# Kernel tuning notes

Measured on AMD Instinct MI355X. Metric: run time of the kernel, lower is better.

Reference implementation:

```python
import jax, jax.numpy as jnp
import numpy as np

B, L, D_IN, D_MODEL, N_LAYERS, D_STATE, D_OUT = 32, 1024, 3, 512, 4, 64, 10


def setup_inputs() -> dict:
    key = jax.random.key(0)
    ks = jax.random.split(key, 6)
    x = jax.random.normal(ks[0], (B, L, D_IN), jnp.float32)
    W_enc = jax.random.normal(ks[1], (D_IN, D_MODEL), jnp.float32) / np.sqrt(D_IN)
    # per-channel log timestep, standard S4 init range [1e-3, 1e-1]
    log_dt = jax.random.uniform(ks[2], (N_LAYERS, D_MODEL), jnp.float32,
                                minval=np.log(1e-3), maxval=np.log(1e-1))
    # S4D-real init: A_n = -(n + 1/2), stored as log of magnitude
    A_log = jnp.broadcast_to(
        jnp.log(0.5 + jnp.arange(D_STATE, dtype=jnp.float32)),
        (N_LAYERS, D_MODEL, D_STATE)) * jnp.ones((), jnp.float32)
    C = jax.random.normal(ks[3], (N_LAYERS, D_MODEL, D_STATE), jnp.float32) / np.sqrt(D_STATE)
    W_ff = jax.random.normal(ks[4], (N_LAYERS, D_MODEL, D_MODEL), jnp.float32) / np.sqrt(D_MODEL)
    W_dec = jax.random.normal(ks[5], (D_MODEL, D_OUT), jnp.float32) / np.sqrt(D_MODEL)
    return dict(x=x, W_enc=W_enc, log_dt=log_dt, A_log=A_log, C=C, W_ff=W_ff, W_dec=W_dec)


def _s4d(x, log_dt, A_log, C):
    """Diagonal real S4D layer (is_real=True, skip=False, identity activation).
    x: (B, L, H); log_dt: (H,); A_log, C: (H, N).
    """
    Lx = x.shape[1]
    dt = jnp.exp(log_dt)                         # (H,)
    A = -jnp.exp(A_log)                          # (H, N) real negative poles
    dtA = dt[:, None] * A                        # (H, N)
    Bbar = (jnp.exp(dtA) - 1.0) / A              # ZOH discretization with B = 1
    # Vandermonde kernel: K[h, l] = sum_n (C*Bbar)[h, n] * exp(dtA[h, n] * l)
    lrange = jnp.arange(Lx, dtype=x.dtype)
    K = jnp.einsum('hn,hnl->hl', C * Bbar, jnp.exp(dtA[:, :, None] * lrange))
    # causal depthwise convolution via FFT (linear conv, pad to 2L)
    n = 2 * Lx
    Kf = jnp.fft.rfft(K, n=n, axis=-1)           # (H, n//2+1)
    xf = jnp.fft.rfft(x, n=n, axis=1)            # (B, n//2+1, H)
    y = jnp.fft.irfft(xf * Kf.T[None], n=n, axis=1)[:, :Lx]
    return y


def reference(x, W_enc, log_dt, A_log, C, W_ff, W_dec):
    h = x @ W_enc                                # (B, L, d_model), bias=False
    for i in range(N_LAYERS):
        h = _s4d(h, log_dt[i], A_log[i], C[i])   # S4D layer
        # dropout is identity at inference; FF block: Linear(no bias) + ReLU
        h = jax.nn.relu(h @ W_ff[i])
    out = h @ W_dec                              # (B, L, d_output)
    return out[:, -1, :]                         # get_last=True -> (B, d_output)
```

## Files before the change

kernel.cpp:

```cpp
#include <hip/hip_runtime.h>
#include <math.h>

#define B_   32
#define L_   1024
#define BT_  (B_*L_)
#define DIN  3
#define H_   512
#define NL   4
#define NS   64
#define DOUT 10
#define CT   128
#define NC   (L_/CT)
#define BH   (B_*H_)

typedef __attribute__((ext_vector_type(8))) _Float16 f16x8;
typedef __attribute__((ext_vector_type(4))) float f32x4;

__device__ inline void gload16(const void* g, void* l) {
    __builtin_amdgcn_global_load_lds((const __attribute__((address_space(1))) void*)g,
                                     (__attribute__((address_space(3))) void*)l, 16, 0, 0);
}

__device__ inline unsigned packh2(float a, float b) {
    unsigned short lo = __builtin_bit_cast(unsigned short, (_Float16)a);
    unsigned short hi = __builtin_bit_cast(unsigned short, (_Float16)b);
    return (unsigned)lo | ((unsigned)hi << 16);
}
__device__ inline float lo16f(unsigned v) {
    return (float)__builtin_bit_cast(_Float16, (unsigned short)(v & 0xffffu));
}
__device__ inline float hi16f(unsigned v) {
    return (float)__builtin_bit_cast(_Float16, (unsigned short)(v >> 16));
}

#define PSW(row, col) ((row) * 64 + ((col) ^ (((row) & 7) << 3)))

#define RAW_BARRIER() do { \
    asm volatile("s_waitcnt lgkmcnt(0)" ::: "memory"); \
    __builtin_amdgcn_s_barrier(); \
    asm volatile("" ::: "memory"); } while (0)

__global__ __launch_bounds__(512, 4) void conv_fused(const float* __restrict__ x,
                                                     const float* __restrict__ Wenc,
                                                     const float* __restrict__ log_dt,
                                                     const float* __restrict__ A_log,
                                                     const float* __restrict__ Cmat,
                                                     const float* __restrict__ WffL,
                                                     _Float16* __restrict__ WTl,
                                                     const _Float16* __restrict__ XT,
                                                     _Float16* __restrict__ YT,
                                                     float* __restrict__ ylast,
                                                     float* __restrict__ outz,
                                                     int layer, int doY) {
    __shared__ __align__(16) _Float16 smem[32768];
    __shared__ float Kl4[4][128];
    __shared__ float Kl[128];
    __shared__ unsigned T32[256];
    __shared__ float dAs[64];
    __shared__ float wps[64];
    __shared__ float rTs[64];
    _Float16* Vl  = smem;
    _Float16* Xh0 = smem + 8192;
    _Float16* Pl  = smem + 16384;
    _Float16* X1r = smem + 24576;
    _Float16* S0l = smem + 24576;
    _Float16* Bp  = smem;

    int bid = blockIdx.x;
    int h = bid >> 1, mh = bid & 1;
    int tid = threadIdx.x;
    int w = tid >> 6, l = tid & 63;
    const int fr = l & 15, q = l >> 4;
    const int wm = w >> 1, wn = w & 1;
    const _Float16* Xh = XT + (size_t)h * BT_ + (size_t)mh * 16384;

    const int c = l & 7, rsub = l >> 3;
    float w0e = 0.f, w1e = 0.f, w2e = 0.f;
    if (layer == 0) { w0e = Wenc[h]; w1e = Wenc[H_ + h]; w2e = Wenc[2 * H_ + h]; }

    if (layer == 0) {
        if (bid == 0 && tid < B_ * DOUT) outz[tid] = 0.f;
#pragma unroll
        for (int s = 0; s < 2; s++) {
            _Float16* dst = s ? X1r : Xh0;
#pragma unroll
            for (int ii = 0; ii < 2; ii++) {
                int t2 = w * 2 + ii;
                int rr = t2 * 8 + rsub;
                int srcc = c ^ (rr & 7);
                int bt = mh * 16384 + rr * 128 + s * 64 + srcc * 8;
                const float* xp = x + (size_t)bt * DIN;
                f16x8 o;
#pragma unroll
                for (int e = 0; e < 8; e++)
                    o[e] = (_Float16)fmaf(xp[e * 3], w0e,
                                     fmaf(xp[e * 3 + 1], w1e, xp[e * 3 + 2] * w2e));
                *(f16x8*)&dst[t2 * 512 + l * 8] = o;
            }
        }
    } else {
#pragma unroll
        for (int s = 0; s < 2; s++) {
            _Float16* dst = s ? X1r : Xh0;
#pragma unroll
            for (int ii = 0; ii < 2; ii++) {
                int t2 = w * 2 + ii;
                int rr = t2 * 8 + rsub;
                int srcc = c ^ (rr & 7);
                gload16(Xh + (size_t)rr * 128 + s * 64 + srcc * 8,
                        &dst[t2 * 512 + l * 8]);
            }
        }
    }

    if (tid < 64) {
        int n = tid;
        float dt  = expf(log_dt[layer * H_ + h]);
        float A   = -expf(A_log[((size_t)layer * H_ + h) * NS + n]);
        float dtA = dt * A;
        float r0  = expf(dtA);
        dAs[n] = dtA;
        wps[n] = Cmat[((size_t)layer * H_ + h) * NS + n] * ((r0 - 1.0f) / A);
        rTs[n] = expf(dtA * (float)CT);
    } else if (layer < 3 && tid < 96) {
        int g = bid * 32 + (tid - 64);
        int n = g >> 6, k8 = g & 63;
        const float* src = WffL + n;
        f16x8 o;
#pragma unroll
        for (int j = 0; j < 8; j++)
            o[j] = (_Float16)src[(size_t)(k8 * 8 + j) * H_];
        *(f16x8*)(WTl + (size_t)n * H_ + k8 * 8) = o;
    }
    RAW_BARRIER();

#pragma unroll
    for (int ii = 0; ii < 2; ii++) {
        int slot = tid + 512 * ii;
        int n = slot >> 4, cc = slot & 15;
        float da = dAs[n];
        int jb = cc * 8;
        float cur  = __expf(da * (float)(127 - jb));
        float rinv = __expf(-da);
        f16x8 vv;
#pragma unroll
        for (int e = 0; e < 8; e++) { vv[e] = (_Float16)cur; cur *= rinv; }
        *(f16x8*)&Vl[n * 128 + ((cc >> 3) * 8 + ((cc & 7) ^ (n & 7))) * 8] = vv;
    }
    if (doY) {
        int t = tid & 127, g = tid >> 7;
        float k = 0.f, d = (float)t;
        for (int n = g * 16; n < g * 16 + 16; n++) k += wps[n] * __expf(dAs[n] * d);
        Kl4[g][t] = k;
    }
    asm volatile("s_waitcnt vmcnt(2) lgkmcnt(0)" ::: "memory");
    __builtin_amdgcn_s_barrier();
    asm volatile("" ::: "memory");

    if (doY && tid < 128)
        Kl[tid] = (Kl4[0][tid] + Kl4[1][tid]) + (Kl4[2][tid] + Kl4[3][tid]);

    f16x8 fA[2][2][2];
    f32x4 accP[2][2] = {};
#pragma unroll
    for (int i = 0; i < 2; i++)
#pragma unroll
        for (int kk = 0; kk < 2; kk++) {
            int row = wm * 32 + i * 16 + fr;
            int kc = kk * 4 + q;
            fA[i][0][kk] = *(const f16x8*)&Xh0[row * 64 + ((kc ^ (row & 7)) * 8)];
        }
#pragma unroll
    for (int kk = 0; kk < 2; kk++) {
        int kc = kk * 4 + q;
        f16x8 bv[2];
#pragma unroll
        for (int j = 0; j < 2; j++) {
            int n = wn * 32 + j * 16 + fr;
            bv[j] = *(const f16x8*)&Vl[n * 128 + 0 * 64 + ((kc ^ (n & 7)) * 8)];
        }
#pragma unroll
        for (int i = 0; i < 2; i++)
#pragma unroll
            for (int j = 0; j < 2; j++)
                accP[i][j] = __builtin_amdgcn_mfma_f32_16x16x32_f16(
                    fA[i][0][kk], bv[j], accP[i][j], 0, 0, 0);
    }

    asm volatile("s_waitcnt vmcnt(0) lgkmcnt(0)" ::: "memory");
    __builtin_amdgcn_s_barrier();
    asm volatile("" ::: "memory");

#pragma unroll
    for (int i = 0; i < 2; i++)
#pragma unroll
        for (int kk = 0; kk < 2; kk++) {
            int row = wm * 32 + i * 16 + fr;
            int kc = kk * 4 + q;
            fA[i][1][kk] = *(const f16x8*)&X1r[row * 64 + ((kc ^ (row & 7)) * 8)];
        }
#pragma unroll
    for (int kk = 0; kk < 2; kk++) {
        int kc = kk * 4 + q;
        f16x8 bv[2];
#pragma unroll
        for (int j = 0; j < 2; j++) {
            int n = wn * 32 + j * 16 + fr;
            bv[j] = *(const f16x8*)&Vl[n * 128 + 1 * 64 + ((kc ^ (n & 7)) * 8)];
        }
#pragma unroll
        for (int i = 0; i < 2; i++)
#pragma unroll
            for (int j = 0; j < 2; j++)
                accP[i][j] = __builtin_amdgcn_mfma_f32_16x16x32_f16(
                    fA[i][1][kk], bv[j], accP[i][j], 0, 0, 0);
    }

#pragma unroll
    for (int i = 0; i < 2; i++)
#pragma unroll
        for (int j = 0; j < 2; j++)
#pragma unroll
            for (int tt = 0; tt < 4; tt++) {
                int row = wm * 32 + i * 16 + q * 4 + tt;
                int col = wn * 32 + j * 16 + fr;
                Pl[PSW(row, col)] = (_Float16)accP[i][j][tt];
            }
    __syncthreads();

    if (doY && tid < 256) {
        int d = tid - 128;
        unsigned short lo = 0, hi = 0;
        if (d >= 0) lo = __builtin_bit_cast(unsigned short, (_Float16)Kl[d]);
        if (d >= 1) hi = __builtin_bit_cast(unsigned short, (_Float16)Kl[d - 1]);
        T32[tid] = (unsigned)lo | ((unsigned)hi << 16);
    }

    {
        int bl = tid >> 5, n0 = (tid & 31) * 2;
        float rT0 = rTs[n0], rT1 = rTs[n0 + 1];
        float E0 = 0.f, E1 = 0.f;
        if (doY) {
#pragma unroll
            for (int cc = 0; cc < 8; cc++) {
                int row = bl * 8 + cc;
                *(unsigned*)&S0l[row * 64 + (((n0 >> 3) ^ (row & 7)) * 8) + (n0 & 7)] =
                    packh2(E0, E1);
                unsigned pv = *(const unsigned*)&Pl[PSW(row, n0)];
                E0 = fmaf(rT0, E0, lo16f(pv));
                E1 = fmaf(rT1, E1, hi16f(pv));
            }
        } else {
#pragma unroll
            for (int cc = 0; cc < 8; cc++) {
                int row = bl * 8 + cc;
                unsigned pv = *(const unsigned*)&Pl[PSW(row, n0)];
                E0 = fmaf(rT0, E0, lo16f(pv));
                E1 = fmaf(rT1, E1, hi16f(pv));
            }
            float wE = fmaf(wps[n0], E0, wps[n0 + 1] * E1);
            wE += __shfl_xor(wE, 16);
            wE += __shfl_xor(wE, 8);  wE += __shfl_xor(wE, 4);
            wE += __shfl_xor(wE, 2);  wE += __shfl_xor(wE, 1);
            if ((l & 31) == 0) ylast[(size_t)(mh * 16 + bl) * H_ + h] = wE;
        }
    }
    if (!doY) return;
    __syncthreads();

    {
        int n0 = (tid & 31) * 2, tc = tid >> 5;
        int t0 = tc * 8;
        float ra0 = __expf(dAs[n0]),     ra1 = __expf(dAs[n0 + 1]);
        float c0  = wps[n0] * __expf(dAs[n0] * (float)(t0 + 1));
        float c1  = wps[n0 + 1] * __expf(dAs[n0 + 1] * (float)(t0 + 1));
#pragma unroll
        for (int e = 0; e < 8; e++) {
            *(unsigned*)&Bp[(t0 + e) * 192 + (16 + ((n0 >> 3) ^ e)) * 8 + (n0 & 7)] =
                packh2(c0, c1);
            c0 *= ra0; c1 *= ra1;
        }
    }
#pragma unroll
    for (int ii = 0; ii < 4; ii++) {
        int slot = tid + 512 * ii;
        int t = slot >> 4, cc = slot & 15;
        unsigned* bp32 = (unsigned*)&Bp[t * 192 + ((cc >> 3) * 8 + ((cc & 7) ^ (t & 7))) * 8];
        int base = t - cc * 8 + 128;
#pragma unroll
        for (int p = 0; p < 4; p++)
            bp32[p] = T32[base - 2 * p];
    }
    __syncthreads();

    f32x4 acc[2][4] = {};
#pragma unroll
    for (int s = 0; s < 3; s++)
#pragma unroll
        for (int kk = 0; kk < 2; kk++) {
            int kc = kk * 4 + q;
            f16x8 av[2], bv[4];
#pragma unroll
            for (int i = 0; i < 2; i++) {
                int row = wm * 32 + i * 16 + fr;
                av[i] = (s < 2) ? fA[i][s][kk]
                                : *(const f16x8*)&S0l[row * 64 + ((kc ^ (row & 7)) * 8)];
            }
#pragma unroll
            for (int j = 0; j < 4; j++) {
                int tc = wn * 64 + j * 16 + fr;
                bv[j] = *(const f16x8*)&Bp[tc * 192 + (s * 8 + (kc ^ (tc & 7))) * 8];
            }
#pragma unroll
            for (int i = 0; i < 2; i++)
#pragma unroll
                for (int j = 0; j < 4; j++)
                    acc[i][j] = __builtin_amdgcn_mfma_f32_16x16x32_f16(av[i], bv[j], acc[i][j], 0, 0, 0);
        }

    __syncthreads();
#pragma unroll
    for (int i = 0; i < 2; i++)
#pragma unroll
        for (int j = 0; j < 4; j++)
#pragma unroll
            for (int tt = 0; tt < 4; tt++) {
                int row = wm * 32 + i * 16 + q * 4 + tt;
                int col = wn * 64 + j * 16 + fr;
                smem[row * 136 + col] = (_Float16)acc[i][j][tt];
            }
    __syncthreads();
    _Float16* Yp = YT + (size_t)h * BT_ + (size_t)mh * 16384;
#pragma unroll
    for (int k2 = 0; k2 < 4; k2++) {
        int ch = tid + 512 * k2;
        int r = ch >> 4, c8 = ch & 15;
        *(f16x8*)(Yp + (size_t)r * 128 + c8 * 8) = *(const f16x8*)&smem[r * 136 + c8 * 8];
    }
}

__global__ __launch_bounds__(512, 4) void ffn_gemm_T(
    const _Float16* __restrict__ WT,
    const _Float16* __restrict__ YT,
    _Float16* __restrict__ OT)
{
    __shared__ __align__(16) _Float16 pool[29184];
    _Float16* As0 = pool;
    _Float16* Bs0 = pool + 12288;
    const int tid = threadIdx.x;
    const int l = tid & 63, w = tid >> 6;
    const int bid = blockIdx.x;
    const int xcd = bid & 7, slot = bid >> 3;
    const int bt0 = (xcd * 16 + (slot >> 2)) * 256;
    const int bn  = (slot & 3) * 128;
    const int srow = l >> 2, schunk = (l & 3) ^ ((l >> 3) & 3);
    const _Float16* ga0 = WT + (size_t)(bn + w * 16 + srow) * H_ + schunk * 8;
    const int btg = tid & 15, kp = (tid >> 4) & 15, bth = tid >> 8;
    const _Float16* gb = YT + (size_t)(kp * 2) * BT_ + bt0 + bth * 128 + btg * 8;

    f16x8 stB[2][2];
    f32x4 acc[4][4] = {};

    auto loadB = [&](int ks, int st) {
        stB[st][0] = *(const f16x8*)(gb + (size_t)(ks * 32) * BT_);
        stB[st][1] = *(const f16x8*)(gb + (size_t)(ks * 32 + 1) * BT_);
    };
    auto stageA = [&](int ks, int buf) {
        gload16(ga0 + ks * 32, As0 + buf * 4096 + w * 512);
    };
    auto writeB = [&](int st, int buf) {
        const int kpc = kp >> 2, kps = kp & 3;
#pragma unroll
        for (int e = 0; e < 8; e++) {
            int row = bth * 128 + btg * 8 + e;
            int off = row * 32 + (row >> 3) * 8 + ((kpc ^ ((row >> 1) & 3)) * 8) + kps * 2;
            _Float16 lo = stB[st][0][e], hi = stB[st][1][e];
            unsigned v = (unsigned)__builtin_bit_cast(unsigned short, lo)
                       | ((unsigned)__builtin_bit_cast(unsigned short, hi) << 16);
            *(unsigned*)&Bs0[buf * 8448 + off] = v;
        }
    };

    loadB(0, 0);
    loadB(1, 1);
    __builtin_amdgcn_sched_barrier(0);
    stageA(0, 0);
    stageA(1, 1);
    writeB(0, 0);
    asm volatile("s_waitcnt vmcnt(1) lgkmcnt(0)" ::: "memory");
    __builtin_amdgcn_s_barrier();
    asm volatile("" ::: "memory");

    const int wm = w >> 2, wn = w & 3;
    const int fr = l & 15, q = l >> 4;
    const int axor = ((fr >> 1) & 3);
#pragma unroll
    for (int ks = 0; ks < 16; ks++) {
        const int a_cur = ks % 3;
        const int b_cur = ks & 1;
        if (ks + 2 < 16) {
            loadB(ks + 2, b_cur);
            __builtin_amdgcn_sched_barrier(0);
            stageA(ks + 2, (ks + 2) % 3);
        }
        f16x8 av[4], bv[4];
#pragma unroll
        for (int i = 0; i < 4; i++) {
            int row = wm * 64 + i * 16 + fr;
            av[i] = *(const f16x8*)&As0[a_cur * 4096 + row * 32 + ((q ^ axor) * 8)];
        }
#pragma unroll
        for (int j = 0; j < 4; j++) {
            int row = wn * 64 + j * 16 + fr;
            bv[j] = *(const f16x8*)&Bs0[b_cur * 8448 + row * 32 + (row >> 3) * 8
                                        + ((q ^ ((row >> 1) & 3)) * 8)];
        }
#pragma unroll
        for (int i = 0; i < 4; i++)
#pragma unroll
            for (int j = 0; j < 4; j++)
                acc[i][j] = __builtin_amdgcn_mfma_f32_16x16x32_f16(av[i], bv[j], acc[i][j], 0, 0, 0);
        if (ks + 1 < 16) {
            writeB((ks + 1) & 1, b_cur ^ 1);
            if (ks + 2 < 16)
                asm volatile("s_waitcnt vmcnt(3) lgkmcnt(0)" ::: "memory");
            else
                asm volatile("s_waitcnt vmcnt(0) lgkmcnt(0)" ::: "memory");
            __builtin_amdgcn_s_barrier();
            asm volatile("" ::: "memory");
        }
    }
    asm volatile("s_waitcnt lgkmcnt(0)" ::: "memory");
    __builtin_amdgcn_s_barrier();
    asm volatile("" ::: "memory");

#pragma unroll
    for (int half = 0; half < 2; half++) {
        if (half) __syncthreads();
        if (wm == half) {
#pragma unroll
            for (int i = 0; i < 4; i++)
#pragma unroll
                for (int j = 0; j < 4; j++)
#pragma unroll
                    for (int tt = 0; tt < 4; tt++) {
                        int r  = i * 16 + q * 4 + tt;
                        int cc = wn * 64 + j * 16 + fr;
                        pool[r * 264 + cc] = (_Float16)fmaxf(acc[i][j][tt], 0.f);
                    }
        }
        __syncthreads();
#pragma unroll
        for (int k2 = 0; k2 < 4; k2++) {
            int ch = tid + 512 * k2;
            int r = ch >> 5, c8 = ch & 31;
            *(f16x8*)(OT + (size_t)(bn + half * 64 + r) * BT_ + bt0 + c8 * 8) =
                *(const f16x8*)&pool[r * 264 + c8 * 8];
        }
    }
}

__global__ __launch_bounds__(512) void final_head2(const float* __restrict__ ylast,
                                                   const float* __restrict__ Wff3,
                                                   const float* __restrict__ Wdec,
                                                   float* __restrict__ out) {
    int bid = blockIdx.x;
    int b = bid >> 3, s = bid & 7;
    int tid = threadIdx.x;
    __shared__ float yrow[H_];
    __shared__ float hpart[8][64];
    yrow[tid] = ylast[(size_t)b * H_ + tid];
    __syncthreads();
    int kg = tid >> 6, tl = tid & 63;
    int t = s * 64 + tl;
    float acc = 0.f;
    const float* wcol = Wff3 + t;
    for (int k = kg * 64; k < kg * 64 + 64; k++)
        acc = fmaf(yrow[k], wcol[(size_t)k * H_], acc);
    hpart[kg][tl] = acc;
    __syncthreads();
    if (tid < 64) {
        float hv = 0.f;
#pragma unroll
        for (int g = 0; g < 8; g++) hv += hpart[g][tid];
        hv = fmaxf(hv, 0.f);
#pragma unroll
        for (int d = 0; d < DOUT; d++) {
            float v = hv * Wdec[(size_t)(s * 64 + tid) * DOUT + d];
            v += __shfl_xor(v, 32); v += __shfl_xor(v, 16);
            v += __shfl_xor(v, 8);  v += __shfl_xor(v, 4);
            v += __shfl_xor(v, 2);  v += __shfl_xor(v, 1);
            if (tid == 0) atomicAdd(&out[(size_t)b * DOUT + d], v);
        }
    }
}

extern "C" void kernel_launch(void* const* d_in, const int* in_sizes, int n_in,
                              void* d_out, int out_size, void* d_ws, size_t ws_size,
                              hipStream_t stream) {
    const float* x      = (const float*)d_in[0];
    const float* Wenc   = (const float*)d_in[1];
    const float* log_dt = (const float*)d_in[2];
    const float* A_log  = (const float*)d_in[3];
    const float* Cmat   = (const float*)d_in[4];
    const float* Wff    = (const float*)d_in[5];
    const float* Wdec   = (const float*)d_in[6];
    float* out = (float*)d_out;

    char* ws = (char*)d_ws;
    _Float16* bufA  = (_Float16*)(ws);
    _Float16* bufB  = (_Float16*)(ws + 33554432);
    _Float16* WT    = (_Float16*)(ws + 68681728);
    float*    ylast = (float*)(ws + 70254592);

    for (int l = 0; l < NL; l++) {
        if (l < NL - 1) {
            conv_fused<<<H_ * 2, 512, 0, stream>>>(x, Wenc, log_dt, A_log, Cmat,
                                                   Wff + (size_t)l * H_ * H_,
                                                   WT + (size_t)l * H_ * H_,
                                                   bufA, bufB, ylast, out, l, 1);
            ffn_gemm_T<<<512, 512, 0, stream>>>(
                WT + (size_t)l * H_ * H_, bufB, bufA);
        } else {
            conv_fused<<<H_ * 2, 512, 0, stream>>>(x, Wenc, log_dt, A_log, Cmat,
                                                   Wff + (size_t)l * H_ * H_,
                                                   WT,
                                                   bufA, bufB, ylast, out, l, 0);
            final_head2<<<B_ * 8, 512, 0, stream>>>(ylast, Wff + (size_t)l * H_ * H_, Wdec, out);
        }
    }
}
```

Before: 176.1 us.

## Process both batch halves per block in conv kernel with prefetch overlap

```diff
diff --git a/kernel.cpp b/kernel.cpp
--- a/kernel.cpp
+++ b/kernel.cpp
@@ -59,36 +59,33 @@
     __shared__ float dAs[64];
     __shared__ float wps[64];
     __shared__ float rTs[64];
-    _Float16* Vl  = smem;
-    _Float16* Xh0 = smem + 8192;
+    _Float16* X0l = smem;
+    _Float16* Vl  = smem + 8192;
     _Float16* Pl  = smem + 16384;
-    _Float16* X1r = smem + 24576;
+    _Float16* X1l = smem + 24576;
     _Float16* S0l = smem + 24576;
     _Float16* Bp  = smem;
-
-    int bid = blockIdx.x;
-    int h = bid >> 1, mh = bid & 1;
-    int tid = threadIdx.x;
-    int w = tid >> 6, l = tid & 63;
+    _Float16* Et  = smem + 15360;
+
+    const int h = blockIdx.x;
+    const int tid = threadIdx.x;
+    const int w = tid >> 6, l = tid & 63;
     const int fr = l & 15, q = l >> 4;
     const int wm = w >> 1, wn = w & 1;
-    const _Float16* Xh = XT + (size_t)h * BT_ + (size_t)mh * 16384;
-
     const int c = l & 7, rsub = l >> 3;
+
     float w0e = 0.f, w1e = 0.f, w2e = 0.f;
     if (layer == 0) { w0e = Wenc[h]; w1e = Wenc[H_ + h]; w2e = Wenc[2 * H_ + h]; }
 
-    if (layer == 0) {
-        if (bid == 0 && tid < B_ * DOUT) outz[tid] = 0.f;
-#pragma unroll
-        for (int s = 0; s < 2; s++) {
-            _Float16* dst = s ? X1r : Xh0;
+    auto stageHalf = [&](int u, int s) {
+        _Float16* dst = s ? X1l : X0l;
+        if (layer == 0) {
 #pragma unroll
             for (int ii = 0; ii < 2; ii++) {
                 int t2 = w * 2 + ii;
                 int rr = t2 * 8 + rsub;
                 int srcc = c ^ (rr & 7);
-                int bt = mh * 16384 + rr * 128 + s * 64 + srcc * 8;
+                int bt = u * 16384 + rr * 128 + s * 64 + srcc * 8;
                 const float* xp = x + (size_t)bt * DIN;
                 f16x8 o;
 #pragma unroll
@@ -97,21 +94,22 @@
                                      fmaf(xp[e * 3 + 1], w1e, xp[e * 3 + 2] * w2e));
                 *(f16x8*)&dst[t2 * 512 + l * 8] = o;
             }
-        }
-    } else {
-#pragma unroll
-        for (int s = 0; s < 2; s++) {
-            _Float16* dst = s ? X1r : Xh0;
+        } else {
+            const _Float16* Xu = XT + (size_t)h * BT_ + (size_t)u * 16384;
 #pragma unroll
             for (int ii = 0; ii < 2; ii++) {
                 int t2 = w * 2 + ii;
                 int rr = t2 * 8 + rsub;
                 int srcc = c ^ (rr & 7);
-                gload16(Xh + (size_t)rr * 128 + s * 64 + srcc * 8,
+                gload16(Xu + (size_t)rr * 128 + s * 64 + srcc * 8,
                         &dst[t2 * 512 + l * 8]);
             }
         }
-    }
+    };
+
+    stageHalf(0, 0);
+    stageHalf(0, 1);
+    if (layer == 0 && h == 0 && tid < B_ * DOUT) outz[tid] = 0.f;
 
     if (tid < 64) {
         int n = tid;
@@ -122,8 +120,8 @@
         dAs[n] = dtA;
         wps[n] = Cmat[((size_t)layer * H_ + h) * NS + n] * ((r0 - 1.0f) / A);
         rTs[n] = expf(dtA * (float)CT);
-    } else if (layer < 3 && tid < 96) {
-        int g = bid * 32 + (tid - 64);
+    } else if (layer < 3 && tid < 128) {
+        int g = h * 64 + (tid - 64);
         int n = g >> 6, k8 = g & 63;
         const float* src = WffL + n;
         f16x8 o;
@@ -134,208 +132,221 @@
     }
     RAW_BARRIER();
 
-#pragma unroll
-    for (int ii = 0; ii < 2; ii++) {
-        int slot = tid + 512 * ii;
-        int n = slot >> 4, cc = slot & 15;
-        float da = dAs[n];
-        int jb = cc * 8;
-        float cur  = __expf(da * (float)(127 - jb));
-        float rinv = __expf(-da);
-        f16x8 vv;
-#pragma unroll
-        for (int e = 0; e < 8; e++) { vv[e] = (_Float16)cur; cur *= rinv; }
-        *(f16x8*)&Vl[n * 128 + ((cc >> 3) * 8 + ((cc & 7) ^ (n & 7))) * 8] = vv;
-    }
-    if (doY) {
-        int t = tid & 127, g = tid >> 7;
-        float k = 0.f, d = (float)t;
-        for (int n = g * 16; n < g * 16 + 16; n++) k += wps[n] * __expf(dAs[n] * d);
-        Kl4[g][t] = k;
-    }
-    asm volatile("s_waitcnt vmcnt(2) lgkmcnt(0)" ::: "memory");
-    __builtin_amdgcn_s_barrier();
-    asm volatile("" ::: "memory");
-
-    if (doY && tid < 128)
-        Kl[tid] = (Kl4[0][tid] + Kl4[1][tid]) + (Kl4[2][tid] + Kl4[3][tid]);
-
-    f16x8 fA[2][2][2];
-    f32x4 accP[2][2] = {};
-#pragma unroll
-    for (int i = 0; i < 2; i++)
-#pragma unroll
-        for (int kk = 0; kk < 2; kk++) {
-            int row = wm * 32 + i * 16 + fr;
-            int kc = kk * 4 + q;
-            fA[i][0][kk] = *(const f16x8*)&Xh0[row * 64 + ((kc ^ (row & 7)) * 8)];
-        }
-#pragma unroll
-    for (int kk = 0; kk < 2; kk++) {
-        int kc = kk * 4 + q;
-        f16x8 bv[2];
-#pragma unroll
-        for (int j = 0; j < 2; j++) {
-            int n = wn * 32 + j * 16 + fr;
-            bv[j] = *(const f16x8*)&Vl[n * 128 + 0 * 64 + ((kc ^ (n & 7)) * 8)];
-        }
+    for (int u = 0; u < 2; u++) {
+#pragma unroll
+        for (int ii = 0; ii < 2; ii++) {
+            int slot = tid + 512 * ii;
+            int n = slot >> 4, cc = slot & 15;
+            float da = dAs[n];
+            int jb = cc * 8;
+            float cur  = __expf(da * (float)(127 - jb));
+            float rinv = __expf(-da);
+            f16x8 vv;
+#pragma unroll
+            for (int e = 0; e < 8; e++) { vv[e] = (_Float16)cur; cur *= rinv; }
+            *(f16x8*)&Vl[n * 128 + ((cc >> 3) * 8 + ((cc & 7) ^ (n & 7))) * 8] = vv;
+        }
+        if (u == 0 && doY) {
+            int t = tid & 127, g = tid >> 7;
+            float k = 0.f, d = (float)t;
+            for (int n = g * 16; n < g * 16 + 16; n++) k += wps[n] * __expf(dAs[n] * d);
+            Kl4[g][t] = k;
+        }
+        asm volatile("s_waitcnt vmcnt(2) lgkmcnt(0)" ::: "memory");
+        __builtin_amdgcn_s_barrier();
+        asm volatile("" ::: "memory");
+
+        if (u == 0 && doY && tid < 128)
+            Kl[tid] = (Kl4[0][tid] + Kl4[1][tid]) + (Kl4[2][tid] + Kl4[3][tid]);
+
+        f16x8 fA[2][2][2];
+        f32x4 accP[2][2] = {};
 #pragma unroll
         for (int i = 0; i < 2; i++)
 #pragma unroll
-            for (int j = 0; j < 2; j++)
-                accP[i][j] = __builtin_amdgcn_mfma_f32_16x16x32_f16(
-                    fA[i][0][kk], bv[j], accP[i][j], 0, 0, 0);
-    }
-
-    asm volatile("s_waitcnt vmcnt(0) lgkmcnt(0)" ::: "memory");
-    __builtin_amdgcn_s_barrier();
-    asm volatile("" ::: "memory");
-
-#pragma unroll
-    for (int i = 0; i < 2; i++)
-#pragma unroll
-        for (int kk = 0; kk < 2; kk++) {
-            int row = wm * 32 + i * 16 + fr;
-            int kc = kk * 4 + q;
-            fA[i][1][kk] = *(const f16x8*)&X1r[row * 64 + ((kc ^ (row & 7)) * 8)];
-        }
-#pragma unroll
-    for (int kk = 0; kk < 2; kk++) {
-        int kc = kk * 4 + q;
-        f16x8 bv[2];
-#pragma unroll
-        for (int j = 0; j < 2; j++) {
-            int n = wn * 32 + j * 16 + fr;
-            bv[j] = *(const f16x8*)&Vl[n * 128 + 1 * 64 + ((kc ^ (n & 7)) * 8)];
-        }
-#pragma unroll
-        for (int i = 0; i < 2; i++)
-#pragma unroll
-            for (int j = 0; j < 2; j++)
-                accP[i][j] = __builtin_amdgcn_mfma_f32_16x16x32_f16(
-                    fA[i][1][kk], bv[j], accP[i][j], 0, 0, 0);
-    }
-
-#pragma unroll
-    for (int i = 0; i < 2; i++)
-#pragma unroll
-        for (int j = 0; j < 2; j++)
-#pragma unroll
-            for (int tt = 0; tt < 4; tt++) {
-                int row = wm * 32 + i * 16 + q * 4 + tt;
-                int col = wn * 32 + j * 16 + fr;
-                Pl[PSW(row, col)] = (_Float16)accP[i][j][tt];
-            }
-    __syncthreads();
-
-    if (doY && tid < 256) {
-        int d = tid - 128;
-        unsigned short lo = 0, hi = 0;
-        if (d >= 0) lo = __builtin_bit_cast(unsigned short, (_Float16)Kl[d]);
-        if (d >= 1) hi = __builtin_bit_cast(unsigned short, (_Float16)Kl[d - 1]);
-        T32[tid] = (unsigned)lo | ((unsigned)hi << 16);
-    }
-
-    {
-        int bl = tid >> 5, n0 = (tid & 31) * 2;
-        float rT0 = rTs[n0], rT1 = rTs[n0 + 1];
-        float E0 = 0.f, E1 = 0.f;
-        if (doY) {
-#pragma unroll
-            for (int cc = 0; cc < 8; cc++) {
-                int row = bl * 8 + cc;
-                *(unsigned*)&S0l[row * 64 + (((n0 >> 3) ^ (row & 7)) * 8) + (n0 & 7)] =
-                    packh2(E0, E1);
-                unsigned pv = *(const unsigned*)&Pl[PSW(row, n0)];
-                E0 = fmaf(rT0, E0, lo16f(pv));
-                E1 = fmaf(rT1, E1, hi16f(pv));
-            }
-        } else {
-#pragma unroll
-            for (int cc = 0; cc < 8; cc++) {
-                int row = bl * 8 + cc;
-                unsigned pv = *(const unsigned*)&Pl[PSW(row, n0)];
-                E0 = fmaf(rT0, E0, lo16f(pv));
-                E1 = fmaf(rT1, E1, hi16f(pv));
-            }
-            float wE = fmaf(wps[n0], E0, wps[n0 + 1] * E1);
-            wE += __shfl_xor(wE, 16);
-            wE += __shfl_xor(wE, 8);  wE += __shfl_xor(wE, 4);
-            wE += __shfl_xor(wE, 2);  wE += __shfl_xor(wE, 1);
-            if ((l & 31) == 0) ylast[(size_t)(mh * 16 + bl) * H_ + h] = wE;
-        }
-    }
-    if (!doY) return;
-    __syncthreads();
-
-    {
-        int n0 = (tid & 31) * 2, tc = tid >> 5;
-        int t0 = tc * 8;
-        float ra0 = __expf(dAs[n0]),     ra1 = __expf(dAs[n0 + 1]);
-        float c0  = wps[n0] * __expf(dAs[n0] * (float)(t0 + 1));
-        float c1  = wps[n0 + 1] * __expf(dAs[n0 + 1] * (float)(t0 + 1));
-#pragma unroll
-        for (int e = 0; e < 8; e++) {
-            *(unsigned*)&Bp[(t0 + e) * 192 + (16 + ((n0 >> 3) ^ e)) * 8 + (n0 & 7)] =
-                packh2(c0, c1);
-            c0 *= ra0; c1 *= ra1;
-        }
-    }
-#pragma unroll
-    for (int ii = 0; ii < 4; ii++) {
-        int slot = tid + 512 * ii;
-        int t = slot >> 4, cc = slot & 15;
-        unsigned* bp32 = (unsigned*)&Bp[t * 192 + ((cc >> 3) * 8 + ((cc & 7) ^ (t & 7))) * 8];
-        int base = t - cc * 8 + 128;
-#pragma unroll
-        for (int p = 0; p < 4; p++)
-            bp32[p] = T32[base - 2 * p];
-    }
-    __syncthreads();
-
-    f32x4 acc[2][4] = {};
-#pragma unroll
-    for (int s = 0; s < 3; s++)
+            for (int kk = 0; kk < 2; kk++) {
+                int row = wm * 32 + i * 16 + fr;
+                int kc = kk * 4 + q;
+                fA[i][0][kk] = *(const f16x8*)&X0l[row * 64 + ((kc ^ (row & 7)) * 8)];
+            }
 #pragma unroll
         for (int kk = 0; kk < 2; kk++) {
             int kc = kk * 4 + q;
-            f16x8 av[2], bv[4];
-#pragma unroll
-            for (int i = 0; i < 2; i++) {
+            f16x8 bv[2];
+#pragma unroll
+            for (int j = 0; j < 2; j++) {
+                int n = wn * 32 + j * 16 + fr;
+                bv[j] = *(const f16x8*)&Vl[n * 128 + 0 * 64 + ((kc ^ (n & 7)) * 8)];
+            }
+#pragma unroll
+            for (int i = 0; i < 2; i++)
+#pragma unroll
+                for (int j = 0; j < 2; j++)
+                    accP[i][j] = __builtin_amdgcn_mfma_f32_16x16x32_f16(
+                        fA[i][0][kk], bv[j], accP[i][j], 0, 0, 0);
+        }
+
+        asm volatile("s_waitcnt vmcnt(0) lgkmcnt(0)" ::: "memory");
+        __builtin_amdgcn_s_barrier();
+        asm volatile("" ::: "memory");
+
+#pragma unroll
+        for (int i = 0; i < 2; i++)
+#pragma unroll
+            for (int kk = 0; kk < 2; kk++) {
                 int row = wm * 32 + i * 16 + fr;
-                av[i] = (s < 2) ? fA[i][s][kk]
-                                : *(const f16x8*)&S0l[row * 64 + ((kc ^ (row & 7)) * 8)];
-            }
-#pragma unroll
-            for (int j = 0; j < 4; j++) {
-                int tc = wn * 64 + j * 16 + fr;
-                bv[j] = *(const f16x8*)&Bp[tc * 192 + (s * 8 + (kc ^ (tc & 7))) * 8];
+                int kc = kk * 4 + q;
+                fA[i][1][kk] = *(const f16x8*)&X1l[row * 64 + ((kc ^ (row & 7)) * 8)];
+            }
+#pragma unroll
+        for (int kk = 0; kk < 2; kk++) {
+            int kc = kk * 4 + q;
+            f16x8 bv[2];
+#pragma unroll
+            for (int j = 0; j < 2; j++) {
+                int n = wn * 32 + j * 16 + fr;
+                bv[j] = *(const f16x8*)&Vl[n * 128 + 1 * 64 + ((kc ^ (n & 7)) * 8)];
             }
 #pragma unroll
             for (int i = 0; i < 2; i++)
 #pragma unroll
-                for (int j = 0; j < 4; j++)
-                    acc[i][j] = __builtin_amdgcn_mfma_f32_16x16x32_f16(av[i], bv[j], acc[i][j], 0, 0, 0);
-        }
-
-    __syncthreads();
-#pragma unroll
-    for (int i = 0; i < 2; i++)
-#pragma unroll
-        for (int j = 0; j < 4; j++)
-#pragma unroll
-            for (int tt = 0; tt < 4; tt++) {
-                int row = wm * 32 + i * 16 + q * 4 + tt;
-                int col = wn * 64 + j * 16 + fr;
-                smem[row * 136 + col] = (_Float16)acc[i][j][tt];
-            }
-    __syncthreads();
-    _Float16* Yp = YT + (size_t)h * BT_ + (size_t)mh * 16384;
-#pragma unroll
-    for (int k2 = 0; k2 < 4; k2++) {
-        int ch = tid + 512 * k2;
-        int r = ch >> 4, c8 = ch & 15;
-        *(f16x8*)(Yp + (size_t)r * 128 + c8 * 8) = *(const f16x8*)&smem[r * 136 + c8 * 8];
+                for (int j = 0; j < 2; j++)
+                    accP[i][j] = __builtin_amdgcn_mfma_f32_16x16x32_f16(
+                        fA[i][1][kk], bv[j], accP[i][j], 0, 0, 0);
+        }
+
+#pragma unroll
+        for (int i = 0; i < 2; i++)
+#pragma unroll
+            for (int j = 0; j < 2; j++)
+#pragma unroll
+                for (int tt = 0; tt < 4; tt++) {
+                    int row = wm * 32 + i * 16 + q * 4 + tt;
+                    int col = wn * 32 + j * 16 + fr;
+                    Pl[PSW(row, col)] = (_Float16)accP[i][j][tt];
+                }
+        __syncthreads();
+
+        if (u == 0 && doY && tid < 256) {
+            int d = tid - 128;
+            unsigned short lo = 0, hi = 0;
+            if (d >= 0) lo = __builtin_bit_cast(unsigned short, (_Float16)Kl[d]);
+            if (d >= 1) hi = __builtin_bit_cast(unsigned short, (_Float16)Kl[d - 1]);
+            T32[tid] = (unsigned)lo | ((unsigned)hi << 16);
+        }
+
+        {
+            int bl = tid >> 5, n0 = (tid & 31) * 2;
+            float rT0 = rTs[n0], rT1 = rTs[n0 + 1];
+            float E0 = 0.f, E1 = 0.f;
+            if (doY) {
+#pragma unroll
+                for (int cc = 0; cc < 8; cc++) {
+                    int row = bl * 8 + cc;
+                    *(unsigned*)&S0l[row * 64 + (((n0 >> 3) ^ (row & 7)) * 8) + (n0 & 7)] =
+                        packh2(E0, E1);
+                    unsigned pv = *(const unsigned*)&Pl[PSW(row, n0)];
+                    E0 = fmaf(rT0, E0, lo16f(pv));
+                    E1 = fmaf(rT1, E1, hi16f(pv));
+                }
+            } else {
+#pragma unroll
+                for (int cc = 0; cc < 8; cc++) {
+                    int row = bl * 8 + cc;
+                    unsigned pv = *(const unsigned*)&Pl[PSW(row, n0)];
+                    E0 = fmaf(rT0, E0, lo16f(pv));
+                    E1 = fmaf(rT1, E1, hi16f(pv));
+                }
+                float wE = fmaf(wps[n0], E0, wps[n0 + 1] * E1);
+                wE += __shfl_xor(wE, 16);
+                wE += __shfl_xor(wE, 8);  wE += __shfl_xor(wE, 4);
+                wE += __shfl_xor(wE, 2);  wE += __shfl_xor(wE, 1);
+                if ((l & 31) == 0) ylast[(size_t)(u * 16 + bl) * H_ + h] = wE;
+            }
+        }
+        if (!doY) {
+            if (u == 0) {
+                RAW_BARRIER();
+                stageHalf(1, 0);
+                stageHalf(1, 1);
+            }
+            continue;
+        }
+        __syncthreads();
+
+        {
+            int n0 = (tid & 31) * 2, tc = tid >> 5;
+            int t0 = tc * 8;
+            float ra0 = __expf(dAs[n0]),     ra1 = __expf(dAs[n0 + 1]);
+            float c0  = wps[n0] * __expf(dAs[n0] * (float)(t0 + 1));
+            float c1  = wps[n0 + 1] * __expf(dAs[n0 + 1] * (float)(t0 + 1));
+#pragma unroll
+            for (int e = 0; e < 8; e++) {
+                *(unsigned*)&Bp[(t0 + e) * 192 + (16 + ((n0 >> 3) ^ e)) * 8 + (n0 & 7)] =
+                    packh2(c0, c1);
+                c0 *= ra0; c1 *= ra1;
+            }
+        }
+#pragma unroll
+        for (int ii = 0; ii < 4; ii++) {
+            int slot = tid + 512 * ii;
+            int t = slot >> 4, cc = slot & 15;
+            unsigned* bp32 = (unsigned*)&Bp[t * 192 + ((cc >> 3) * 8 + ((cc & 7) ^ (t & 7))) * 8];
+            int base = t - cc * 8 + 128;
+#pragma unroll
+            for (int p = 0; p < 4; p++)
+                bp32[p] = T32[base - 2 * p];
+        }
+        __syncthreads();
+
+        f32x4 acc[2][4] = {};
+#pragma unroll
+        for (int s = 0; s < 3; s++)
+#pragma unroll
+            for (int kk = 0; kk < 2; kk++) {
+                int kc = kk * 4 + q;
+                f16x8 av[2], bv[4];
+#pragma unroll
+                for (int i = 0; i < 2; i++) {
+                    int row = wm * 32 + i * 16 + fr;
+                    av[i] = (s < 2) ? fA[i][s][kk]
+                                    : *(const f16x8*)&S0l[row * 64 + ((kc ^ (row & 7)) * 8)];
+                }
+#pragma unroll
+                for (int j = 0; j < 4; j++) {
+                    int tc = wn * 64 + j * 16 + fr;
+                    bv[j] = *(const f16x8*)&Bp[tc * 192 + (s * 8 + (kc ^ (tc & 7))) * 8];
+                }
+#pragma unroll
+                for (int i = 0; i < 2; i++)
+#pragma unroll
+                    for (int j = 0; j < 4; j++)
+                        acc[i][j] = __builtin_amdgcn_mfma_f32_16x16x32_f16(
+                            av[i], bv[j], acc[i][j], 0, 0, 0);
+            }
+
+        __syncthreads();
+#pragma unroll
+        for (int i = 0; i < 2; i++)
+#pragma unroll
+            for (int j = 0; j < 4; j++)
+#pragma unroll
+                for (int tt = 0; tt < 4; tt++) {
+                    int row = wm * 32 + i * 16 + q * 4 + tt;
+                    int col = wn * 64 + j * 16 + fr;
+                    Et[row * 136 + col] = (_Float16)acc[i][j][tt];
+                }
+        __syncthreads();
+        if (u == 0) stageHalf(1, 0);
+        _Float16* Yp = YT + (size_t)h * BT_ + (size_t)u * 16384;
+#pragma unroll
+        for (int k2 = 0; k2 < 4; k2++) {
+            int ch = tid + 512 * k2;
+            int r = ch >> 4, c8 = ch & 15;
+            *(f16x8*)(Yp + (size_t)r * 128 + c8 * 8) = *(const f16x8*)&Et[r * 136 + c8 * 8];
+        }
+        RAW_BARRIER();
+        if (u == 0) stageHalf(1, 1);
     }
 }
 
@@ -515,17 +526,17 @@
 
     for (int l = 0; l < NL; l++) {
         if (l < NL - 1) {
-            conv_fused<<<H_ * 2, 512, 0, stream>>>(x, Wenc, log_dt, A_log, Cmat,
-                                                   Wff + (size_t)l * H_ * H_,
-                                                   WT + (size_t)l * H_ * H_,
-                                                   bufA, bufB, ylast, out, l, 1);
+            conv_fused<<<H_, 512, 0, stream>>>(x, Wenc, log_dt, A_log, Cmat,
+                                               Wff + (size_t)l * H_ * H_,
+                                               WT + (size_t)l * H_ * H_,
+                                               bufA, bufB, ylast, out, l, 1);
             ffn_gemm_T<<<512, 512, 0, stream>>>(
                 WT + (size_t)l * H_ * H_, bufB, bufA);
         } else {
-            conv_fused<<<H_ * 2, 512, 0, stream>>>(x, Wenc, log_dt, A_log, Cmat,
-                                                   Wff + (size_t)l * H_ * H_,
-                                                   WT,
-                                                   bufA, bufB, ylast, out, l, 0);
+            conv_fused<<<H_, 512, 0, stream>>>(x, Wenc, log_dt, A_log, Cmat,
+                                               Wff + (size_t)l * H_ * H_,
+                                               WT,
+                                               bufA, bufB, ylast, out, l, 0);
             final_head2<<<B_ * 8, 512, 0, stream>>>(ylast, Wff + (size_t)l * H_ * H_, Wdec, out);
         }
     }
```

After: 263.9 us. 49.9% more time.

## Reshape FFN GEMM tile to 256x128 with double-buffered A staging

Applied to the files above, without the earlier changes.

```diff
diff --git a/kernel.cpp b/kernel.cpp
--- a/kernel.cpp
+++ b/kernel.cpp
@@ -344,19 +344,21 @@
     const _Float16* __restrict__ YT,
     _Float16* __restrict__ OT)
 {
-    __shared__ __align__(16) _Float16 pool[29184];
+    __shared__ __align__(16) _Float16 pool[24832];
     _Float16* As0 = pool;
-    _Float16* Bs0 = pool + 12288;
+    _Float16* Bs0 = pool + 16384;
     const int tid = threadIdx.x;
     const int l = tid & 63, w = tid >> 6;
     const int bid = blockIdx.x;
     const int xcd = bid & 7, slot = bid >> 3;
-    const int bt0 = (xcd * 16 + (slot >> 2)) * 256;
-    const int bn  = (slot & 3) * 128;
+    const int bt0 = (xcd * 32 + (slot >> 1)) * 128;
+    const int bn  = (slot & 1) * 256;
     const int srow = l >> 2, schunk = (l & 3) ^ ((l >> 3) & 3);
-    const _Float16* ga0 = WT + (size_t)(bn + w * 16 + srow) * H_ + schunk * 8;
-    const int btg = tid & 15, kp = (tid >> 4) & 15, bth = tid >> 8;
-    const _Float16* gb = YT + (size_t)(kp * 2) * BT_ + bt0 + bth * 128 + btg * 8;
+    const _Float16* ga0 = WT + (size_t)(bn + (w * 2 + 0) * 16 + srow) * H_ + schunk * 8;
+    const _Float16* ga1 = WT + (size_t)(bn + (w * 2 + 1) * 16 + srow) * H_ + schunk * 8;
+    const int btg = tid & 15, kp = (tid >> 4) & 15;
+    const bool bw = (w < 4);
+    const _Float16* gb = YT + (size_t)(kp * 2) * BT_ + bt0 + btg * 8;
 
     f16x8 stB[2][2];
     f32x4 acc[4][4] = {};
@@ -366,53 +368,56 @@
         stB[st][1] = *(const f16x8*)(gb + (size_t)(ks * 32 + 1) * BT_);
     };
     auto stageA = [&](int ks, int buf) {
-        gload16(ga0 + ks * 32, As0 + buf * 4096 + w * 512);
+        gload16(ga0 + ks * 32, As0 + buf * 8192 + (w * 2 + 0) * 512);
+        gload16(ga1 + ks * 32, As0 + buf * 8192 + (w * 2 + 1) * 512);
     };
     auto writeB = [&](int st, int buf) {
         const int kpc = kp >> 2, kps = kp & 3;
 #pragma unroll
         for (int e = 0; e < 8; e++) {
-            int row = bth * 128 + btg * 8 + e;
+            int row = btg * 8 + e;
             int off = row * 32 + (row >> 3) * 8 + ((kpc ^ ((row >> 1) & 3)) * 8) + kps * 2;
             _Float16 lo = stB[st][0][e], hi = stB[st][1][e];
             unsigned v = (unsigned)__builtin_bit_cast(unsigned short, lo)
                        | ((unsigned)__builtin_bit_cast(unsigned short, hi) << 16);
-            *(unsigned*)&Bs0[buf * 8448 + off] = v;
+            *(unsigned*)&Bs0[buf * 4224 + off] = v;
         }
     };
 
-    loadB(0, 0);
-    loadB(1, 1);
+    if (bw) loadB(0, 0);
     __builtin_amdgcn_sched_barrier(0);
     stageA(0, 0);
-    stageA(1, 1);
-    writeB(0, 0);
-    asm volatile("s_waitcnt vmcnt(1) lgkmcnt(0)" ::: "memory");
+    __builtin_amdgcn_sched_barrier(0);
+    if (bw) {
+        loadB(1, 1);
+        writeB(0, 0);
+        asm volatile("s_waitcnt vmcnt(2) lgkmcnt(0)" ::: "memory");
+    } else {
+        asm volatile("s_waitcnt vmcnt(0) lgkmcnt(0)" ::: "memory");
+    }
     __builtin_amdgcn_s_barrier();
     asm volatile("" ::: "memory");
 
-    const int wm = w >> 2, wn = w & 3;
+    const int wm = w >> 1, wn = w & 1;
     const int fr = l & 15, q = l >> 4;
     const int axor = ((fr >> 1) & 3);
 #pragma unroll
     for (int ks = 0; ks < 16; ks++) {
-        const int a_cur = ks % 3;
+        const int a_cur = ks & 1;
         const int b_cur = ks & 1;
-        if (ks + 2 < 16) {
-            loadB(ks + 2, b_cur);
-            __builtin_amdgcn_sched_barrier(0);
-            stageA(ks + 2, (ks + 2) % 3);
-        }
+        if (ks + 1 < 16) stageA(ks + 1, (ks + 1) & 1);
+        __builtin_amdgcn_sched_barrier(0);
+        if (bw && ks + 2 < 16) loadB(ks + 2, b_cur);
         f16x8 av[4], bv[4];
 #pragma unroll
         for (int i = 0; i < 4; i++) {
             int row = wm * 64 + i * 16 + fr;
-            av[i] = *(const f16x8*)&As0[a_cur * 4096 + row * 32 + ((q ^ axor) * 8)];
+            av[i] = *(const f16x8*)&As0[a_cur * 8192 + row * 32 + ((q ^ axor) * 8)];
         }
 #pragma unroll
         for (int j = 0; j < 4; j++) {
             int row = wn * 64 + j * 16 + fr;
-            bv[j] = *(const f16x8*)&Bs0[b_cur * 8448 + row * 32 + (row >> 3) * 8
+            bv[j] = *(const f16x8*)&Bs0[b_cur * 4224 + row * 32 + (row >> 3) * 8
                                         + ((q ^ ((row >> 1) & 3)) * 8)];
         }
 #pragma unroll
@@ -421,9 +426,9 @@
             for (int j = 0; j < 4; j++)
                 acc[i][j] = __builtin_amdgcn_mfma_f32_16x16x32_f16(av[i], bv[j], acc[i][j], 0, 0, 0);
         if (ks + 1 < 16) {
-            writeB((ks + 1) & 1, b_cur ^ 1);
-            if (ks + 2 < 16)
-                asm volatile("s_waitcnt vmcnt(3) lgkmcnt(0)" ::: "memory");
+            if (bw) writeB((ks + 1) & 1, b_cur ^ 1);
+            if (bw && ks + 2 < 16)
+                asm volatile("s_waitcnt vmcnt(2) lgkmcnt(0)" ::: "memory");
             else
                 asm volatile("s_waitcnt vmcnt(0) lgkmcnt(0)" ::: "memory");
             __builtin_amdgcn_s_barrier();
@@ -435,9 +440,9 @@
     asm volatile("" ::: "memory");
 
 #pragma unroll
-    for (int half = 0; half < 2; half++) {
-        if (half) __syncthreads();
-        if (wm == half) {
+    for (int qt = 0; qt < 4; qt++) {
+        if (qt) __syncthreads();
+        if (wm == qt) {
 #pragma unroll
             for (int i = 0; i < 4; i++)
 #pragma unroll
@@ -446,16 +451,16 @@
                     for (int tt = 0; tt < 4; tt++) {
                         int r  = i * 16 + q * 4 + tt;
                         int cc = wn * 64 + j * 16 + fr;
-                        pool[r * 264 + cc] = (_Float16)fmaxf(acc[i][j][tt], 0.f);
+                        pool[r * 136 + cc] = (_Float16)fmaxf(acc[i][j][tt], 0.f);
                     }
         }
         __syncthreads();
 #pragma unroll
-        for (int k2 = 0; k2 < 4; k2++) {
+        for (int k2 = 0; k2 < 2; k2++) {
             int ch = tid + 512 * k2;
-            int r = ch >> 5, c8 = ch & 31;
-            *(f16x8*)(OT + (size_t)(bn + half * 64 + r) * BT_ + bt0 + c8 * 8) =
-                *(const f16x8*)&pool[r * 264 + c8 * 8];
+            int r = ch >> 4, c8 = ch & 15;
+            *(f16x8*)(OT + (size_t)(bn + qt * 64 + r) * BT_ + bt0 + c8 * 8) =
+                *(const f16x8*)&pool[r * 136 + c8 * 8];
         }
     }
 }
```

Result: slower. 183.5 us (+4.2%).
